# Kernel tuning notes

Hardware: AMD Instinct MI355X
Metric: run time of the kernel (lower is better)

The kernel has to match this reference:

```python
import jax, jax.numpy as jnp
import numpy as np

B, N, H, K = 8192, 256, 2048, 1
BETA = 0.99
LOG2PI = float(np.log(2.0 * np.pi))


def V(z, Wv):
    # quadratic Lyapunov-style function; one positive value per sample (keepdims)
    u = z @ Wv
    return jnp.sum(u * u, axis=-1, keepdims=True) + 1e-3


def setup_inputs() -> dict:
    key = jax.random.key(0)
    ks = jax.random.split(key, 6)
    s1 = 1.0 / np.sqrt(N)
    s2 = 1.0 / np.sqrt(H)
    return {
        "x": jax.random.normal(ks[0], (B, N), jnp.float32),
        "y": jax.random.normal(ks[1], (B, 1, N), jnp.float32),
        "eps": jax.random.normal(ks[2], (B, 1, N), jnp.float32),
        "W1": jax.random.normal(ks[3], (N, H), jnp.float32) * s1,
        "b1": jnp.zeros((H,), jnp.float32),
        "W2": jax.random.normal(ks[4], (H, 2 * N), jnp.float32) * s2,
        "b2": jnp.zeros((2 * N,), jnp.float32),
        "Wv": jax.random.normal(ks[5], (N, N), jnp.float32) * s1,
    }


def reference(x, y, eps, W1, b1, W2, b2, Wv):
    # fhat: 2-layer MLP -> [B, 2N] = concat(mu, logvar)
    h = jnp.tanh(x @ W1 + b1)
    f = h @ W2 + b2
    mu, logvar = jnp.split(f, 2, axis=-1)            # [B, K*N] each (K=1)
    # torch: stack(split(mu, N, dim=1)).view(-1, 1, N)
    mu = mu.reshape(B, K, N).transpose(1, 0, 2).reshape(B * K, 1, N)
    var = jnp.exp(logvar).reshape(B, K, N).transpose(1, 0, 2).reshape(B * K, 1, N)
    # Lyapunov rescaling of the mean (per-sample scalar scale)
    Vx = V(x, Wv)[:, None, :]                        # [B,1,1]
    Vmu = V(mu, Wv)                                  # [B,1,1]
    bVx = BETA * Vx
    mu_stable = mu * ((bVx - jax.nn.relu(bVx - Vmu)) / Vmu)
    # reparameterized sample of diagonal MVN
    fx = mu_stable + jnp.sqrt(var) * eps             # [B,1,N]
    # diagonal-MVN log_prob, single fused pass
    q = (y - mu_stable) ** 2 / var
    logp = -0.5 * (N * LOG2PI + jnp.sum(jnp.log(var) + q, axis=-1))  # [B,1]
    logp_y = -jnp.sum(logp)
    return fx, logp_y
```

## Files before the change

### kernel.cpp

```cpp
#include <hip/hip_runtime.h>
#include <stdint.h>

#define B_SZ 8192
#define N_SZ 256
#define H_SZ 2048
#define LOG2PI_F 1.8378770664093453f
#define BETA_F 0.99f

typedef unsigned short ushort_t;
typedef __attribute__((ext_vector_type(8))) __bf16 bf16x8;
typedef __attribute__((ext_vector_type(4))) float f32x4;
typedef __attribute__((ext_vector_type(8))) ushort_t u16x8;

__device__ __forceinline__ ushort_t f2bf(float f) {
    unsigned int u = __float_as_uint(f);
    unsigned int r = (u + 0x7FFFu + ((u >> 16) & 1u)) >> 16;
    return (ushort_t)r;
}

__device__ __forceinline__ float fast_tanh(float v) {
    float ex = __expf(2.0f * v);
    return 1.0f - __fdividef(2.0f, ex + 1.0f);
}

__device__ __forceinline__ void async_ld16(const void* g, const char* lds_uniform) {
    __builtin_amdgcn_global_load_lds(
        (const __attribute__((address_space(1))) void*)g,
        (__attribute__((address_space(3))) void*)lds_uniform,
        16, 0, 0);
}

__global__ __launch_bounds__(256, 4)
void gemm1_kernel(const ushort_t* __restrict__ xb, const ushort_t* __restrict__ W1p,
                  const float* __restrict__ b1, ushort_t* __restrict__ hp)
{
    __shared__ __align__(16) char smem[34816];
    char* sA = smem;
    char* sB = smem + 16384;
    const int tid = threadIdx.x;
    const int lane = tid & 63;
    const int w = tid >> 6;
    const int q = lane >> 4;
    const int rlo = lane & 15;
    const int wr = w >> 1, wc = w & 1;

    const int bid = blockIdx.x;
    const int r8 = bid & 7;
    const int u = bid >> 3;
    const int cb = u & 15;
    const int tb = u >> 4;
    const int row0 = (r8 + 8 * tb) * 128;
    const int n0 = cb * 128;

    f32x4 acc[4][4];
#pragma unroll
    for (int i = 0; i < 4; ++i)
#pragma unroll
        for (int j = 0; j < 4; ++j)
            acc[i][j] = f32x4{0.f, 0.f, 0.f, 0.f};

    for (int k0 = 0; k0 < N_SZ; k0 += 64) {
        __syncthreads();
#pragma unroll
        for (int r = 0; r < 4; ++r) {
            int c = r * 256 + tid;
            int kq = c >> 7, m = c & 127;
            async_ld16(xb + (size_t)(row0 + m) * N_SZ + k0 + kq * 8, sA + (c << 4));
        }
        int ko0 = k0 >> 3;
#pragma unroll
        for (int r = 0; r < 4; ++r) {
            int c = r * 256 + tid;
            int kq = c >> 7, n = c & 127;
            async_ld16(W1p + ((size_t)(ko0 + kq) * H_SZ + n0 + n) * 8, sB + (c << 4));
        }
        __syncthreads();

#pragma unroll
        for (int ks = 0; ks < 2; ++ks) {
            int kq = ks * 4 + q;
            bf16x8 af[4], bfr[4];
#pragma unroll
            for (int i = 0; i < 4; ++i)
                af[i] = *(const bf16x8*)(sA + (((kq << 7) + wr * 64 + i * 16 + rlo) << 4));
#pragma unroll
            for (int j = 0; j < 4; ++j)
                bfr[j] = *(const bf16x8*)(sB + (((kq << 7) + wc * 64 + j * 16 + rlo) << 4));
#pragma unroll
            for (int i = 0; i < 4; ++i)
#pragma unroll
                for (int j = 0; j < 4; ++j)
                    acc[i][j] = __builtin_amdgcn_mfma_f32_16x16x32_bf16(af[i], bfr[j], acc[i][j], 0, 0, 0);
        }
    }

    __syncthreads();
    ushort_t* st = (ushort_t*)smem;
#pragma unroll
    for (int j = 0; j < 4; ++j) {
        int coll = wc * 64 + j * 16 + rlo;
        float bv = b1[n0 + coll];
#pragma unroll
        for (int i = 0; i < 4; ++i) {
            int rowl = wr * 64 + i * 16 + q * 4;
#pragma unroll
            for (int rr = 0; rr < 4; ++rr)
                st[(rowl + rr) * 136 + coll] = f2bf(fast_tanh(acc[i][j][rr] + bv));
        }
    }
    __syncthreads();
#pragma unroll
    for (int r = 0; r < 8; ++r) {
        int c = r * 256 + tid;
        int m = c & 127, ko = c >> 7;
        u16x8 v = *(const u16x8*)(st + m * 136 + ko * 8);
        *(u16x8*)(hp + ((size_t)((n0 >> 3) + ko) * B_SZ + row0 + m) * 8) = v;
    }
}

__global__ __launch_bounds__(256, 2)
void gemm2_kernel(const ushort_t* __restrict__ hp, const ushort_t* __restrict__ W2p,
                  const float* __restrict__ b2, float* __restrict__ f,
                  ushort_t* __restrict__ mub)
{
    __shared__ __align__(16) char smem[49152];
    char* sA = smem;
    char* sB = smem + 16384;
    const int tid = threadIdx.x;
    const int lane = tid & 63;
    const int w = tid >> 6;
    const int q = lane >> 4;
    const int rlo = lane & 15;
    const int wr = w >> 1, wc = w & 1;

    const int bid = blockIdx.x;
    const int r8 = bid & 7;
    const int u = bid >> 3;
    const int cb = u & 3;
    const int tb = u >> 2;
    const int row0 = (r8 + 8 * tb) * 64;
    const int n0 = cb * 128;

    f32x4 acc[2][4];
#pragma unroll
    for (int i = 0; i < 2; ++i)
#pragma unroll
        for (int j = 0; j < 4; ++j)
            acc[i][j] = f32x4{0.f, 0.f, 0.f, 0.f};

    for (int k0 = 0; k0 < H_SZ; k0 += 128) {
        __syncthreads();
        int ko0 = k0 >> 3;
#pragma unroll
        for (int r = 0; r < 4; ++r) {
            int c = r * 256 + tid;
            int kq = c >> 6, m = c & 63;
            async_ld16(hp + ((size_t)(ko0 + kq) * B_SZ + row0 + m) * 8, sA + (c << 4));
        }
#pragma unroll
        for (int r = 0; r < 8; ++r) {
            int c = r * 256 + tid;
            int kq = c >> 7, n = c & 127;
            async_ld16(W2p + ((size_t)(ko0 + kq) * 512 + n0 + n) * 8, sB + (c << 4));
        }
        __syncthreads();

#pragma unroll
        for (int ks = 0; ks < 4; ++ks) {
            int kq = ks * 4 + q;
            bf16x8 af[2], bfr[4];
#pragma unroll
            for (int i = 0; i < 2; ++i)
                af[i] = *(const bf16x8*)(sA + (((kq << 6) + wr * 32 + i * 16 + rlo) << 4));
#pragma unroll
            for (int j = 0; j < 4; ++j)
                bfr[j] = *(const bf16x8*)(sB + (((kq << 7) + wc * 64 + j * 16 + rlo) << 4));
#pragma unroll
            for (int i = 0; i < 2; ++i)
#pragma unroll
                for (int j = 0; j < 4; ++j)
                    acc[i][j] = __builtin_amdgcn_mfma_f32_16x16x32_bf16(af[i], bfr[j], acc[i][j], 0, 0, 0);
        }
    }

#pragma unroll
    for (int j = 0; j < 4; ++j) {
        int col = n0 + wc * 64 + j * 16 + rlo;
        float bv = b2[col];
#pragma unroll
        for (int i = 0; i < 2; ++i) {
            int rowb = row0 + wr * 32 + i * 16 + q * 4;
#pragma unroll
            for (int rr = 0; rr < 4; ++rr)
                f[(size_t)(rowb + rr) * 512 + col] = acc[i][j][rr] + bv;
        }
    }
    if (n0 < N_SZ) {
        __syncthreads();
        ushort_t* st = (ushort_t*)smem;
#pragma unroll
        for (int j = 0; j < 4; ++j) {
            int coll = wc * 64 + j * 16 + rlo;
            float bv = b2[n0 + coll];
#pragma unroll
            for (int i = 0; i < 2; ++i) {
                int rowl = wr * 32 + i * 16 + q * 4;
#pragma unroll
                for (int rr = 0; rr < 4; ++rr)
                    st[(rowl + rr) * 136 + coll] = f2bf(acc[i][j][rr] + bv);
            }
        }
        __syncthreads();
#pragma unroll
        for (int r = 0; r < 4; ++r) {
            int c = r * 256 + tid;
            int m = c >> 4, c8 = c & 15;
            u16x8 v = *(const u16x8*)(st + m * 136 + c8 * 8);
            *(u16x8*)(mub + (size_t)(row0 + m) * N_SZ + n0 + c8 * 8) = v;
        }
    }
}

__global__ __launch_bounds__(256)
void vmu_epilogue_kernel(const ushort_t* __restrict__ xb, const ushort_t* __restrict__ mub,
                         const ushort_t* __restrict__ Wvp,
                         const float* __restrict__ f, const float* __restrict__ y,
                         const float* __restrict__ eps,
                         float* __restrict__ out, float* __restrict__ partials)
{
    __shared__ float vsx[4][16];
    __shared__ float vsm[4][16];
    __shared__ float vxs[16];
    __shared__ float vms[16];
    __shared__ float red[4];
    const int tid = threadIdx.x;
    const int lane = tid & 63;
    const int w = tid >> 6;
    const int q = lane >> 4;
    const int rlo = lane & 15;
    const int r0 = blockIdx.x * 16;

    f32x4 accx[4], accm[4];
#pragma unroll
    for (int j = 0; j < 4; ++j) {
        accx[j] = f32x4{0.f, 0.f, 0.f, 0.f};
        accm[j] = f32x4{0.f, 0.f, 0.f, 0.f};
    }

    const ushort_t* ax = xb + (size_t)(r0 + rlo) * N_SZ + q * 8;
    const ushort_t* am = mub + (size_t)(r0 + rlo) * N_SZ + q * 8;
    const ushort_t* b0 = Wvp + ((size_t)q * N_SZ + w * 64 + rlo) * 8;
#pragma unroll
    for (int s = 0; s < 8; ++s) {
        bf16x8 afx = *(const bf16x8*)(ax + s * 32);
        bf16x8 afm = *(const bf16x8*)(am + s * 32);
        bf16x8 bfr[4];
#pragma unroll
        for (int j = 0; j < 4; ++j)
            bfr[j] = *(const bf16x8*)(b0 + s * 4 * N_SZ * 8 + j * 128);
#pragma unroll
        for (int j = 0; j < 4; ++j) {
            accx[j] = __builtin_amdgcn_mfma_f32_16x16x32_bf16(afx, bfr[j], accx[j], 0, 0, 0);
            accm[j] = __builtin_amdgcn_mfma_f32_16x16x32_bf16(afm, bfr[j], accm[j], 0, 0, 0);
        }
    }
#pragma unroll
    for (int rr = 0; rr < 4; ++rr) {
        float sx = 0.f, sm = 0.f;
#pragma unroll
        for (int j = 0; j < 4; ++j) {
            float vx_ = accx[j][rr]; sx += vx_ * vx_;
            float vm_ = accm[j][rr]; sm += vm_ * vm_;
        }
#pragma unroll
        for (int m = 1; m < 16; m <<= 1) {
            sx += __shfl_xor(sx, m, 64);
            sm += __shfl_xor(sm, m, 64);
        }
        if (rlo == 0) {
            vsx[w][q * 4 + rr] = sx;
            vsm[w][q * 4 + rr] = sm;
        }
    }
    __syncthreads();
    if (tid < 16) {
        vxs[tid] = 1e-3f + vsx[0][tid] + vsx[1][tid] + vsx[2][tid] + vsx[3][tid];
        vms[tid] = 1e-3f + vsm[0][tid] + vsm[1][tid] + vsm[2][tid] + vsm[3][tid];
    }
    __syncthreads();

    float t = 0.f;
    const int n = tid;
#pragma unroll 4
    for (int r = 0; r < 16; ++r) {
        size_t row = (size_t)(r0 + r);
        float mu = f[row * 512 + n];
        float lv = f[row * 512 + 256 + n];
        float var = expf(lv);
        float Vx = vxs[r];
        float Vmu = vms[r];
        float scale = fminf(BETA_F * Vx, Vmu) / Vmu;
        float mus = mu * scale;
        out[row * 256 + n] = mus + sqrtf(var) * eps[row * 256 + n];
        float d = y[row * 256 + n] - mus;
        t += lv + d * d / var;
    }
#pragma unroll
    for (int m = 32; m >= 1; m >>= 1) t += __shfl_down(t, m, 64);
    if (lane == 0) red[w] = t;
    __syncthreads();
    if (tid == 0)
        partials[blockIdx.x] = red[0] + red[1] + red[2] + red[3];
}

__global__ __launch_bounds__(256)
void reduce_kernel(const float* __restrict__ partials, float* __restrict__ out)
{
    int tid = threadIdx.x;
    float s = partials[tid] + partials[tid + 256];
#pragma unroll
    for (int m = 32; m >= 1; m >>= 1) s += __shfl_down(s, m, 64);
    __shared__ float red[4];
    if ((tid & 63) == 0) red[tid >> 6] = s;
    __syncthreads();
    if (tid == 0)
        out[(size_t)B_SZ * N_SZ] =
            0.5f * (red[0] + red[1] + red[2] + red[3] +
                    (float)N_SZ * LOG2PI_F * (float)B_SZ);
}

__global__ __launch_bounds__(256)
void convert_kernel(const float* __restrict__ x, const float* __restrict__ W1,
                    const float* __restrict__ W2, const float* __restrict__ Wv,
                    ushort_t* __restrict__ xb, ushort_t* __restrict__ W1p,
                    ushort_t* __restrict__ W2p, ushort_t* __restrict__ Wvp)
{
    const int XC = 262144, W1C = 65536, W2C = 131072;
    int c = blockIdx.x * 256 + threadIdx.x;
    if (c < XC) {
        f32x4 a = *(const f32x4*)(x + (size_t)c * 8);
        f32x4 b = *(const f32x4*)(x + (size_t)c * 8 + 4);
        u16x8 o;
#pragma unroll
        for (int i = 0; i < 4; ++i) { o[i] = f2bf(a[i]); o[4 + i] = f2bf(b[i]); }
        *(u16x8*)(xb + (size_t)c * 8) = o;
    } else if (c < XC + W1C) {
        int d = c - XC;
        int ko = d >> 11, n = d & 2047;
        u16x8 o;
#pragma unroll
        for (int ki = 0; ki < 8; ++ki)
            o[ki] = f2bf(W1[(size_t)(ko * 8 + ki) * H_SZ + n]);
        *(u16x8*)(W1p + (size_t)d * 8) = o;
    } else if (c < XC + W1C + W2C) {
        int d = c - XC - W1C;
        int ko = d >> 9, n = d & 511;
        u16x8 o;
#pragma unroll
        for (int ki = 0; ki < 8; ++ki)
            o[ki] = f2bf(W2[(size_t)(ko * 8 + ki) * 512 + n]);
        *(u16x8*)(W2p + (size_t)d * 8) = o;
    } else {
        int d = c - XC - W1C - W2C;
        int ko = d >> 8, n = d & 255;
        u16x8 o;
#pragma unroll
        for (int ki = 0; ki < 8; ++ki)
            o[ki] = f2bf(Wv[(size_t)(ko * 8 + ki) * N_SZ + n]);
        *(u16x8*)(Wvp + (size_t)d * 8) = o;
    }
}

extern "C" void kernel_launch(void* const* d_in, const int* in_sizes, int n_in,
                              void* d_out, int out_size, void* d_ws, size_t ws_size,
                              hipStream_t stream)
{
    const float* x   = (const float*)d_in[0];
    const float* y   = (const float*)d_in[1];
    const float* eps = (const float*)d_in[2];
    const float* W1  = (const float*)d_in[3];
    const float* b1  = (const float*)d_in[4];
    const float* W2  = (const float*)d_in[5];
    const float* b2  = (const float*)d_in[6];
    const float* Wv  = (const float*)d_in[7];
    float* out = (float*)d_out;

    char* ws = (char*)d_ws;
    size_t off = 0;
    auto alloc = [&](size_t bytes) {
        char* p = ws + off;
        off += (bytes + 255) & ~(size_t)255;
        return p;
    };
    ushort_t* xb  = (ushort_t*)alloc((size_t)B_SZ * N_SZ * 2);
    ushort_t* W1p = (ushort_t*)alloc((size_t)N_SZ * H_SZ * 2);
    ushort_t* W2p = (ushort_t*)alloc((size_t)H_SZ * 512 * 2);
    ushort_t* Wvp = (ushort_t*)alloc((size_t)N_SZ * N_SZ * 2);
    ushort_t* hp  = (ushort_t*)alloc((size_t)B_SZ * H_SZ * 2);
    float*    f   = (float*)alloc((size_t)B_SZ * 512 * 4);
    ushort_t* mub = (ushort_t*)alloc((size_t)B_SZ * N_SZ * 2);
    float*    partials = (float*)alloc(512 * 4);

    const int TOTALC = 262144 + 65536 + 131072 + 8192;
    convert_kernel<<<TOTALC / 256, 256, 0, stream>>>(x, W1, W2, Wv, xb, W1p, W2p, Wvp);

    gemm1_kernel<<<1024, 256, 0, stream>>>(xb, W1p, b1, hp);
    gemm2_kernel<<<512, 256, 0, stream>>>(hp, W2p, b2, f, mub);
    vmu_epilogue_kernel<<<512, 256, 0, stream>>>(xb, mub, Wvp, f, y, eps, out, partials);
    reduce_kernel<<<1, 256, 0, stream>>>(partials, out);
}
```

Measured before the change: 151.7 us.

## Split-K gemm2 into two halves and fuse partial-sum reduction into epilogue

The second GEMM is split along K into two halves, written to two fp32 partial buffers, and launched with twice as many blocks. The K-tile and shared memory are halved so more blocks fit per CU. The bias add, the sum of the partials and the bf16 conversion of mu move into the Vmu/epilogue kernel, which now reads both partials. This raises parallelism and occupancy for the GEMM, at the cost of extra fp32 traffic for the second partial buffer.

```diff
diff --git a/kernel.cpp b/kernel.cpp
--- a/kernel.cpp
+++ b/kernel.cpp
@@ -118,14 +118,13 @@
     }
 }
 
-__global__ __launch_bounds__(256, 2)
+__global__ __launch_bounds__(256, 4)
 void gemm2_kernel(const ushort_t* __restrict__ hp, const ushort_t* __restrict__ W2p,
-                  const float* __restrict__ b2, float* __restrict__ f,
-                  ushort_t* __restrict__ mub)
-{
-    __shared__ __align__(16) char smem[49152];
+                  float* __restrict__ f01)
+{
+    __shared__ __align__(16) char smem[24576];
     char* sA = smem;
-    char* sB = smem + 16384;
+    char* sB = smem + 8192;
     const int tid = threadIdx.x;
     const int lane = tid & 63;
     const int w = tid >> 6;
@@ -136,10 +135,14 @@
     const int bid = blockIdx.x;
     const int r8 = bid & 7;
     const int u = bid >> 3;
-    const int cb = u & 3;
-    const int tb = u >> 2;
+    const int zb = u & 1;
+    const int v = u >> 1;
+    const int cb = v & 3;
+    const int tb = v >> 2;
     const int row0 = (r8 + 8 * tb) * 64;
     const int n0 = cb * 128;
+    const int kbase = zb * (H_SZ / 2);
+    float* f = f01 + (size_t)zb * B_SZ * 512;
 
     f32x4 acc[2][4];
 #pragma unroll
@@ -148,17 +151,17 @@
         for (int j = 0; j < 4; ++j)
             acc[i][j] = f32x4{0.f, 0.f, 0.f, 0.f};
 
-    for (int k0 = 0; k0 < H_SZ; k0 += 128) {
+    for (int k0 = kbase; k0 < kbase + H_SZ / 2; k0 += 64) {
         __syncthreads();
         int ko0 = k0 >> 3;
 #pragma unroll
-        for (int r = 0; r < 4; ++r) {
+        for (int r = 0; r < 2; ++r) {
             int c = r * 256 + tid;
             int kq = c >> 6, m = c & 63;
             async_ld16(hp + ((size_t)(ko0 + kq) * B_SZ + row0 + m) * 8, sA + (c << 4));
         }
 #pragma unroll
-        for (int r = 0; r < 8; ++r) {
+        for (int r = 0; r < 4; ++r) {
             int c = r * 256 + tid;
             int kq = c >> 7, n = c & 127;
             async_ld16(W2p + ((size_t)(ko0 + kq) * 512 + n0 + n) * 8, sB + (c << 4));
@@ -166,7 +169,7 @@
         __syncthreads();
 
 #pragma unroll
-        for (int ks = 0; ks < 4; ++ks) {
+        for (int ks = 0; ks < 2; ++ks) {
             int kq = ks * 4 + q;
             bf16x8 af[2], bfr[4];
 #pragma unroll
@@ -186,46 +189,20 @@
 #pragma unroll
     for (int j = 0; j < 4; ++j) {
         int col = n0 + wc * 64 + j * 16 + rlo;
-        float bv = b2[col];
 #pragma unroll
         for (int i = 0; i < 2; ++i) {
             int rowb = row0 + wr * 32 + i * 16 + q * 4;
 #pragma unroll
             for (int rr = 0; rr < 4; ++rr)
-                f[(size_t)(rowb + rr) * 512 + col] = acc[i][j][rr] + bv;
-        }
-    }
-    if (n0 < N_SZ) {
-        __syncthreads();
-        ushort_t* st = (ushort_t*)smem;
-#pragma unroll
-        for (int j = 0; j < 4; ++j) {
-            int coll = wc * 64 + j * 16 + rlo;
-            float bv = b2[n0 + coll];
-#pragma unroll
-            for (int i = 0; i < 2; ++i) {
-                int rowl = wr * 32 + i * 16 + q * 4;
-#pragma unroll
-                for (int rr = 0; rr < 4; ++rr)
-                    st[(rowl + rr) * 136 + coll] = f2bf(acc[i][j][rr] + bv);
-            }
-        }
-        __syncthreads();
-#pragma unroll
-        for (int r = 0; r < 4; ++r) {
-            int c = r * 256 + tid;
-            int m = c >> 4, c8 = c & 15;
-            u16x8 v = *(const u16x8*)(st + m * 136 + c8 * 8);
-            *(u16x8*)(mub + (size_t)(row0 + m) * N_SZ + n0 + c8 * 8) = v;
+                f[(size_t)(rowb + rr) * 512 + col] = acc[i][j][rr];
         }
     }
 }
 
 __global__ __launch_bounds__(256)
-void vmu_epilogue_kernel(const ushort_t* __restrict__ xb, const ushort_t* __restrict__ mub,
-                         const ushort_t* __restrict__ Wvp,
-                         const float* __restrict__ f, const float* __restrict__ y,
-                         const float* __restrict__ eps,
+void vmu_epilogue_kernel(const ushort_t* __restrict__ xb, const float* __restrict__ f01,
+                         const ushort_t* __restrict__ Wvp, const float* __restrict__ b2,
+                         const float* __restrict__ y, const float* __restrict__ eps,
                          float* __restrict__ out, float* __restrict__ partials)
 {
     __shared__ float vsx[4][16];
@@ -239,6 +216,7 @@
     const int q = lane >> 4;
     const int rlo = lane & 15;
     const int r0 = blockIdx.x * 16;
+    const size_t FB = (size_t)B_SZ * 512;
 
     f32x4 accx[4], accm[4];
 #pragma unroll
@@ -248,12 +226,26 @@
     }
 
     const ushort_t* ax = xb + (size_t)(r0 + rlo) * N_SZ + q * 8;
-    const ushort_t* am = mub + (size_t)(r0 + rlo) * N_SZ + q * 8;
+    const float* f0a = f01 + (size_t)(r0 + rlo) * 512 + q * 8;
+    const float* f1a = f0a + FB;
+    const float* b2q = b2 + q * 8;
     const ushort_t* b0 = Wvp + ((size_t)q * N_SZ + w * 64 + rlo) * 8;
 #pragma unroll
     for (int s = 0; s < 8; ++s) {
         bf16x8 afx = *(const bf16x8*)(ax + s * 32);
-        bf16x8 afm = *(const bf16x8*)(am + s * 32);
+        f32x4 p0 = *(const f32x4*)(f0a + s * 32);
+        f32x4 p1 = *(const f32x4*)(f0a + s * 32 + 4);
+        f32x4 q0 = *(const f32x4*)(f1a + s * 32);
+        f32x4 q1 = *(const f32x4*)(f1a + s * 32 + 4);
+        f32x4 b0v = *(const f32x4*)(b2q + s * 32);
+        f32x4 b1v = *(const f32x4*)(b2q + s * 32 + 4);
+        u16x8 am;
+#pragma unroll
+        for (int e = 0; e < 4; ++e) {
+            am[e]     = f2bf(p0[e] + q0[e] + b0v[e]);
+            am[4 + e] = f2bf(p1[e] + q1[e] + b1v[e]);
+        }
+        bf16x8 afm = *(const bf16x8*)&am;
         bf16x8 bfr[4];
 #pragma unroll
         for (int j = 0; j < 4; ++j)
@@ -291,11 +283,13 @@
 
     float t = 0.f;
     const int n = tid;
+    const float b2mu = b2[n];
+    const float b2lv = b2[256 + n];
 #pragma unroll 4
     for (int r = 0; r < 16; ++r) {
         size_t row = (size_t)(r0 + r);
-        float mu = f[row * 512 + n];
-        float lv = f[row * 512 + 256 + n];
+        float mu = f01[row * 512 + n] + f01[FB + row * 512 + n] + b2mu;
+        float lv = f01[row * 512 + 256 + n] + f01[FB + row * 512 + 256 + n] + b2lv;
         float var = expf(lv);
         float Vx = vxs[r];
         float Vmu = vms[r];
@@ -397,15 +391,14 @@
     ushort_t* W2p = (ushort_t*)alloc((size_t)H_SZ * 512 * 2);
     ushort_t* Wvp = (ushort_t*)alloc((size_t)N_SZ * N_SZ * 2);
     ushort_t* hp  = (ushort_t*)alloc((size_t)B_SZ * H_SZ * 2);
-    float*    f   = (float*)alloc((size_t)B_SZ * 512 * 4);
-    ushort_t* mub = (ushort_t*)alloc((size_t)B_SZ * N_SZ * 2);
+    float*    f01 = (float*)alloc((size_t)2 * B_SZ * 512 * 4);
     float*    partials = (float*)alloc(512 * 4);
 
     const int TOTALC = 262144 + 65536 + 131072 + 8192;
     convert_kernel<<<TOTALC / 256, 256, 0, stream>>>(x, W1, W2, Wv, xb, W1p, W2p, Wvp);
 
     gemm1_kernel<<<1024, 256, 0, stream>>>(xb, W1p, b1, hp);
-    gemm2_kernel<<<512, 256, 0, stream>>>(hp, W2p, b2, f, mub);
-    vmu_epilogue_kernel<<<512, 256, 0, stream>>>(xb, mub, Wvp, f, y, eps, out, partials);
+    gemm2_kernel<<<1024, 256, 0, stream>>>(hp, W2p, f01);
+    vmu_epilogue_kernel<<<512, 256, 0, stream>>>(xb, f01, Wvp, b2, y, eps, out, partials);
     reduce_kernel<<<1, 256, 0, stream>>>(partials, out);
 }
```

After: 155.0 us. +2.2%, slower.
